# Kernel optimization log

Hardware: AMD Instinct MI355X
Metric: run time of the kernel (lower is better)

The kernel has to match this reference:

```python
import jax, jax.numpy as jnp
import numpy as np

B, M, N = 1, 128, 256          # batch, MSA rows, residues
C_IN, C_PAIR = 256, 128        # rep1d_feat, rep2d_feat
H, C = 8, 32                   # num_heads, attention_num_c
EPS = 1e-5


def layer_norm(x, g, b):
    mu = jnp.mean(x, axis=-1, keepdims=True)
    var = jnp.var(x, axis=-1, keepdims=True)
    return (x - mu) * jax.lax.rsqrt(var + EPS) * g + b


def setup_inputs() -> dict:
    key = jax.random.key(0)
    ks = jax.random.split(key, 10)
    s_in = 1.0 / np.sqrt(C_IN)
    s_pair = 1.0 / np.sqrt(C_PAIR)
    s_hc = 1.0 / np.sqrt(H * C)
    return {
        "x1d": jax.random.normal(ks[0], (B, M, N, C_IN), jnp.float32),
        "x2d": jax.random.normal(ks[1], (B, N, N, C_PAIR), jnp.float32),
        "ln1_g": jnp.ones((C_IN,), jnp.float32),
        "ln1_b": jnp.zeros((C_IN,), jnp.float32),
        "ln2_g": jnp.ones((C_PAIR,), jnp.float32),
        "ln2_b": jnp.zeros((C_PAIR,), jnp.float32),
        "Wq": jax.random.normal(ks[2], (C_IN, H * C), jnp.float32) * s_in,
        "Wk": jax.random.normal(ks[3], (C_IN, H * C), jnp.float32) * s_in,
        "Wv": jax.random.normal(ks[4], (C_IN, H * C), jnp.float32) * s_in,
        "W2d": jax.random.normal(ks[5], (C_PAIR, H), jnp.float32) * s_pair,
        "Wgate": jax.random.normal(ks[6], (C_IN, H * C), jnp.float32) * s_in,
        "bgate": jnp.zeros((H * C,), jnp.float32),
        "Wfinal": jax.random.normal(ks[7], (H * C, C_IN), jnp.float32) * s_hc,
        "bfinal": jnp.zeros((C_IN,), jnp.float32),
    }


def reference(x1d, x2d, ln1_g, ln1_b, ln2_g, ln2_b,
              Wq, Wk, Wv, W2d, Wgate, bgate, Wfinal, bfinal):
    x1 = layer_norm(x1d, ln1_g, ln1_b)                      # [b,m,i,c_in]
    x2 = layer_norm(x2d, ln2_g, ln2_b)                      # [b,i,j,c_pair]
    bias = jnp.einsum('bijp,ph->bhij', x2, W2d)             # [b,h,i,j]

    factor = 1.0 / np.sqrt(C).astype(np.float32)
    q = jnp.einsum('bmid,dhc->bmihc', x1, Wq.reshape(C_IN, H, C)) * factor
    k = jnp.einsum('bmid,dhc->bmihc', x1, Wk.reshape(C_IN, H, C))
    v = jnp.einsum('bmid,dhc->bmihc', x1, Wv.reshape(C_IN, H, C))

    aff = jnp.einsum('bmihc,bmjhc->bmhij', q, k)            # [b,m,h,i,j]
    weights = jax.nn.softmax(aff + bias[:, None], axis=-1)

    gate = jax.nn.sigmoid(
        jnp.einsum('bmid,dhc->bmihc', x1, Wgate.reshape(C_IN, H, C))
        + bgate.reshape(1, 1, 1, H, C))

    out = jnp.einsum('bmhqk,bmkhc->bmqhc', weights, v) * gate
    out = jnp.einsum('bmqhc,hcd->bmqd', out, Wfinal.reshape(H, C, C_IN)) + bfinal
    return out
```

## Files before the change

kernel.cpp:

```cpp
#include <hip/hip_runtime.h>


typedef unsigned short u16;
typedef unsigned int   u32;
typedef __attribute__((ext_vector_type(8))) __bf16 bf16x8;
typedef __attribute__((ext_vector_type(4))) float  f32x4;

#define DEV __device__ __forceinline__

DEV float bf2f(u16 s) {
    u32 u = ((u32)s) << 16;
    float f;
    __builtin_memcpy(&f, &u, 4);
    return f;
}
DEV u16 f2bf(float f) {
    u32 u;
    __builtin_memcpy(&u, &f, 4);
    u = (u + 0x7fffu + ((u >> 16) & 1u)) >> 16;
    return (u16)u;
}

#define GLD_LDS16(gp, lp)                                                           \
    __builtin_amdgcn_global_load_lds(                                               \
        (const __attribute__((address_space(1))) u32*)(const void*)(gp),            \
        (__attribute__((address_space(3))) u32*)(void*)(lp), 16, 0, 0)

__global__ void k_transpose(const float* __restrict__ Wq, const float* __restrict__ Wk,
                            const float* __restrict__ Wv, const float* __restrict__ Wg,
                            const float* __restrict__ Wf,
                            u16* __restrict__ WT, u16* __restrict__ WfT) {
    int idx = blockIdx.x * 256 + threadIdx.x;
    if (idx < 1024 * 256) {
        int gcol = idx >> 8, p = idx & 255;
        int sel = gcol >> 8, c = gcol & 255;
        const float* W = sel == 0 ? Wq : sel == 1 ? Wk : sel == 2 ? Wv : Wg;
        WT[idx] = f2bf(W[p * 256 + c]);
    } else {
        int j = idx - 1024 * 256;
        int d = j >> 8, hc = j & 255;
        WfT[j] = f2bf(Wf[hc * 256 + d]);
    }
}

__global__ __launch_bounds__(256) void k_ln1(const float* __restrict__ x,
                                             const float* __restrict__ gg,
                                             const float* __restrict__ bb,
                                             u16* __restrict__ y) {
    int lane = threadIdx.x & 63, wave = threadIdx.x >> 6;
    int row = blockIdx.x * 4 + wave;
    float4 xv = *(const float4*)(x + row * 256 + lane * 4);
    float v0 = xv.x, v1 = xv.y, v2 = xv.z, v3 = xv.w;
    float s  = v0 + v1 + v2 + v3;
    float s2 = v0*v0 + v1*v1 + v2*v2 + v3*v3;
    #pragma unroll
    for (int msk = 32; msk; msk >>= 1) {
        s  += __shfl_xor(s,  msk, 64);
        s2 += __shfl_xor(s2, msk, 64);
    }
    float mu  = s * (1.0f / 256.0f);
    float var = s2 * (1.0f / 256.0f) - mu * mu;
    float rs  = rsqrtf(var + 1e-5f);
    float4 gv = *(const float4*)(gg + lane * 4);
    float4 bv = *(const float4*)(bb + lane * 4);
    ushort4 o;
    o.x = f2bf((v0 - mu) * rs * gv.x + bv.x);
    o.y = f2bf((v1 - mu) * rs * gv.y + bv.y);
    o.z = f2bf((v2 - mu) * rs * gv.z + bv.z);
    o.w = f2bf((v3 - mu) * rs * gv.w + bv.w);
    *(ushort4*)(y + row * 256 + lane * 4) = o;
}

__global__ __launch_bounds__(256) void k_ln2bias(const float* __restrict__ x2,
                                                 const float* __restrict__ gg,
                                                 const float* __restrict__ bb,
                                                 const float* __restrict__ W2d,
                                                 float* __restrict__ bias) {
    int lane = threadIdx.x & 63, wave = threadIdx.x >> 6;
    int row = blockIdx.x * 4 + wave;
    float2 xv = *(const float2*)(x2 + row * 128 + lane * 2);
    float v0 = xv.x, v1 = xv.y;
    float s = v0 + v1, s2 = v0*v0 + v1*v1;
    #pragma unroll
    for (int msk = 32; msk; msk >>= 1) {
        s  += __shfl_xor(s,  msk, 64);
        s2 += __shfl_xor(s2, msk, 64);
    }
    float mu  = s * (1.0f / 128.0f);
    float var = s2 * (1.0f / 128.0f) - mu * mu;
    float rs  = rsqrtf(var + 1e-5f);
    float2 gv = *(const float2*)(gg + lane * 2);
    float2 bv = *(const float2*)(bb + lane * 2);
    float xn0 = (v0 - mu) * rs * gv.x + bv.x;
    float xn1 = (v1 - mu) * rs * gv.y + bv.y;
    int p0 = lane * 2;
    float4 w0a = *(const float4*)(W2d + p0 * 8);
    float4 w0b = *(const float4*)(W2d + p0 * 8 + 4);
    float4 w1a = *(const float4*)(W2d + (p0 + 1) * 8);
    float4 w1b = *(const float4*)(W2d + (p0 + 1) * 8 + 4);
    float p[8];
    p[0] = xn0 * w0a.x + xn1 * w1a.x;
    p[1] = xn0 * w0a.y + xn1 * w1a.y;
    p[2] = xn0 * w0a.z + xn1 * w1a.z;
    p[3] = xn0 * w0a.w + xn1 * w1a.w;
    p[4] = xn0 * w0b.x + xn1 * w1b.x;
    p[5] = xn0 * w0b.y + xn1 * w1b.y;
    p[6] = xn0 * w0b.z + xn1 * w1b.z;
    p[7] = xn0 * w0b.w + xn1 * w1b.w;
    #pragma unroll
    for (int hh = 0; hh < 8; hh++)
        #pragma unroll
        for (int msk = 32; msk; msk >>= 1)
            p[hh] += __shfl_xor(p[hh], msk, 64);
    if (lane == 0) {
        #pragma unroll
        for (int hh = 0; hh < 8; hh++)
            bias[hh * 65536 + row] = p[hh];
    }
}

DEV void gemm128_core(const u16* __restrict__ X, const u16* __restrict__ WTb,
                      int rowbase, int colbase, int K,
                      u16* As, u16* Bs, f32x4 acc[4][4], int lane, int wave) {
    int l8 = lane & 7, r8 = lane >> 3;
    int gchunk = l8 ^ (r8 & 7);
    int lrow = lane & 15, quad = lane >> 4;
    int wr = (wave >> 1) * 64, wc = (wave & 1) * 64;

    for (int kk = 0; kk < K; kk += 64) {
        #pragma unroll
        for (int i = 0; i < 4; i++) {
            int s = wave * 4 + i;
            const u16* g = X + (rowbase + s * 8 + r8) * K + kk + gchunk * 8;
            GLD_LDS16(g, As + s * 512);
        }
        #pragma unroll
        for (int i = 0; i < 4; i++) {
            int s = wave * 4 + i;
            const u16* g = WTb + (colbase + s * 8 + r8) * K + kk + gchunk * 8;
            GLD_LDS16(g, Bs + s * 512);
        }
        __syncthreads();
        #pragma unroll
        for (int k2 = 0; k2 < 64; k2 += 32) {
            int cidx = (k2 >> 3) + quad;
            bf16x8 af[4], bf[4];
            #pragma unroll
            for (int t = 0; t < 4; t++) {
                int R = wr + t * 16 + lrow;
                af[t] = *(const bf16x8*)(As + R * 64 + ((cidx ^ (R & 7)) << 3));
            }
            #pragma unroll
            for (int t = 0; t < 4; t++) {
                int R = wc + t * 16 + lrow;
                bf[t] = *(const bf16x8*)(Bs + R * 64 + ((cidx ^ (R & 7)) << 3));
            }
            #pragma unroll
            for (int i = 0; i < 4; i++)
                #pragma unroll
                for (int j = 0; j < 4; j++)
                    acc[i][j] = __builtin_amdgcn_mfma_f32_16x16x32_bf16(af[i], bf[j], acc[i][j], 0, 0, 0);
        }
        __syncthreads();
    }
}

__global__ __launch_bounds__(256) void k_qkvg(const u16* __restrict__ X, const u16* __restrict__ WT,
                                              u16* __restrict__ q, u16* __restrict__ kb,
                                              u16* __restrict__ vt, u16* __restrict__ gt,
                                              const float* __restrict__ bgate) {
    __shared__ u16 As[128 * 64];
    __shared__ u16 Bs[128 * 64];
    int lane = threadIdx.x & 63, wave = threadIdx.x >> 6;
    int rowbase = blockIdx.x * 128;
    int colbase = blockIdx.y * 128;
    f32x4 acc[4][4];
    #pragma unroll
    for (int i = 0; i < 4; i++)
        #pragma unroll
        for (int j = 0; j < 4; j++)
            acc[i][j] = (f32x4){0.f, 0.f, 0.f, 0.f};
    gemm128_core(X, WT, rowbase, colbase, 256, As, Bs, acc, lane, wave);
    int lrow = lane & 15, quad = lane >> 4;
    int wrb = rowbase + (wave >> 1) * 64, wcb = colbase + (wave & 1) * 64;
    int which = blockIdx.y >> 1;
    #pragma unroll
    for (int it = 0; it < 4; it++)
        #pragma unroll
        for (int jt = 0; jt < 4; jt++)
            #pragma unroll
            for (int r = 0; r < 4; r++) {
                int grow = wrb + it * 16 + quad * 4 + r;
                int gcol = wcb + jt * 16 + lrow;
                int o = gcol & 255;
                float v = acc[it][jt][r];
                if (which == 0) {
                    q[grow * 256 + o] = f2bf(v * 0.17677669529663687f);
                } else if (which == 1) {
                    kb[grow * 256 + o] = f2bf(v);
                } else if (which == 2) {
                    int mm = grow >> 8, ii = grow & 255;
                    vt[(mm * 256 + o) * 256 + ii] = f2bf(v);
                } else {
                    float z = v + bgate[o];
                    gt[grow * 256 + o] = f2bf(1.0f / (1.0f + __expf(-z)));
                }
            }
}

__global__ __launch_bounds__(256) void k_attn(const u16* __restrict__ q, const u16* __restrict__ kb,
                                              const u16* __restrict__ vt, const u16* __restrict__ gt,
                                              const float* __restrict__ bias,
                                              u16* __restrict__ tmp) {
    __shared__ u16 P[4][16][264];
    int lane = threadIdx.x & 63, wave = threadIdx.x >> 6;
    int lrow = lane & 15, quad = lane >> 4, lk = quad * 8;
    int m = blockIdx.x, h = blockIdx.y, iblk = blockIdx.z;
    int i0 = iblk * 64 + wave * 16;

    bf16x8 aq = *(const bf16x8*)(q + (m * 256 + i0 + lrow) * 256 + h * 32 + lk);
    f32x4 acc[16];
    #pragma unroll
    for (int jt = 0; jt < 16; jt++) {
        bf16x8 bk = *(const bf16x8*)(kb + (m * 256 + jt * 16 + lrow) * 256 + h * 32 + lk);
        f32x4 z = {0.f, 0.f, 0.f, 0.f};
        acc[jt] = __builtin_amdgcn_mfma_f32_16x16x32_bf16(aq, bk, z, 0, 0, 0);
    }

    float rmax[4] = {-1e30f, -1e30f, -1e30f, -1e30f};
    #pragma unroll
    for (int jt = 0; jt < 16; jt++)
        #pragma unroll
        for (int r = 0; r < 4; r++) {
            int i = i0 + quad * 4 + r;
            int j = jt * 16 + lrow;
            float a = acc[jt][r] + bias[h * 65536 + i * 256 + j];
            acc[jt][r] = a;
            rmax[r] = fmaxf(rmax[r], a);
        }
    #pragma unroll
    for (int r = 0; r < 4; r++)
        #pragma unroll
        for (int msk = 8; msk; msk >>= 1)
            rmax[r] = fmaxf(rmax[r], __shfl_xor(rmax[r], msk, 64));
    float rsum[4] = {0.f, 0.f, 0.f, 0.f};
    #pragma unroll
    for (int jt = 0; jt < 16; jt++)
        #pragma unroll
        for (int r = 0; r < 4; r++) {
            float e = __expf(acc[jt][r] - rmax[r]);
            acc[jt][r] = e;
            rsum[r] += e;
        }
    #pragma unroll
    for (int r = 0; r < 4; r++) {
        #pragma unroll
        for (int msk = 8; msk; msk >>= 1)
            rsum[r] += __shfl_xor(rsum[r], msk, 64);
        rsum[r] = 1.0f / fmaxf(rsum[r], 1e-30f);
    }

    #pragma unroll
    for (int jt = 0; jt < 16; jt++)
        #pragma unroll
        for (int r = 0; r < 4; r++)
            P[wave][quad * 4 + r][jt * 16 + lrow] = f2bf(acc[jt][r] * rsum[r]);
    __syncthreads();

    f32x4 oacc[2] = {{0.f,0.f,0.f,0.f}, {0.f,0.f,0.f,0.f}};
    const u16* Pw = &P[wave][0][0];
    for (int kk2 = 0; kk2 < 256; kk2 += 32) {
        bf16x8 ap = *(const bf16x8*)(Pw + lrow * 264 + kk2 + lk);
        #pragma unroll
        for (int ct = 0; ct < 2; ct++) {
            bf16x8 bv = *(const bf16x8*)(vt + (m * 256 + h * 32 + ct * 16 + lrow) * 256 + kk2 + lk);
            oacc[ct] = __builtin_amdgcn_mfma_f32_16x16x32_bf16(ap, bv, oacc[ct], 0, 0, 0);
        }
    }

    #pragma unroll
    for (int ct = 0; ct < 2; ct++)
        #pragma unroll
        for (int r = 0; r < 4; r++) {
            int i = i0 + quad * 4 + r;
            int o = h * 32 + ct * 16 + lrow;
            float gv = bf2f(gt[(m * 256 + i) * 256 + o]);
            tmp[(m * 256 + i) * 256 + o] = f2bf(oacc[ct][r] * gv);
        }
}

__global__ __launch_bounds__(256) void k_final(const u16* __restrict__ T, const u16* __restrict__ WfT,
                                               const float* __restrict__ bfinal, float* __restrict__ out) {
    __shared__ u16 As[128 * 64];
    __shared__ u16 Bs[128 * 64];
    int lane = threadIdx.x & 63, wave = threadIdx.x >> 6;
    int rowbase = blockIdx.x * 128;
    int colbase = blockIdx.y * 128;
    f32x4 acc[4][4];
    #pragma unroll
    for (int i = 0; i < 4; i++)
        #pragma unroll
        for (int j = 0; j < 4; j++)
            acc[i][j] = (f32x4){0.f, 0.f, 0.f, 0.f};
    gemm128_core(T, WfT, rowbase, colbase, 256, As, Bs, acc, lane, wave);
    int lrow = lane & 15, quad = lane >> 4;
    int wrb = rowbase + (wave >> 1) * 64, wcb = colbase + (wave & 1) * 64;
    #pragma unroll
    for (int it = 0; it < 4; it++)
        #pragma unroll
        for (int jt = 0; jt < 4; jt++)
            #pragma unroll
            for (int r = 0; r < 4; r++) {
                int grow = wrb + it * 16 + quad * 4 + r;
                int gcol = wcb + jt * 16 + lrow;
                out[grow * 256 + gcol] = acc[it][jt][r] + bfinal[gcol];
            }
}

extern "C" void kernel_launch(void* const* d_in, const int* in_sizes, int n_in,
                              void* d_out, int out_size, void* d_ws, size_t ws_size,
                              hipStream_t stream) {
    const float* x1d   = (const float*)d_in[0];
    const float* x2d   = (const float*)d_in[1];
    const float* ln1_g = (const float*)d_in[2];
    const float* ln1_b = (const float*)d_in[3];
    const float* ln2_g = (const float*)d_in[4];
    const float* ln2_b = (const float*)d_in[5];
    const float* Wq    = (const float*)d_in[6];
    const float* Wk    = (const float*)d_in[7];
    const float* Wv    = (const float*)d_in[8];
    const float* W2d   = (const float*)d_in[9];
    const float* Wg    = (const float*)d_in[10];
    const float* bg    = (const float*)d_in[11];
    const float* Wf    = (const float*)d_in[12];
    const float* bfin  = (const float*)d_in[13];
    float* out = (float*)d_out;

    char* ws = (char*)d_ws;
    u16*   x1   = (u16*)(ws);
    u16*   WT   = (u16*)(ws + 16777216);
    u16*   WfT  = (u16*)(ws + 17301504);
    float* bias = (float*)(ws + 17432576);
    u16*   qb   = (u16*)(ws + 19529728);
    u16*   kb   = (u16*)(ws + 36306944);
    u16*   vtb  = (u16*)(ws + 53084160);
    u16*   gb   = (u16*)(ws + 69861376);
    u16*   tmp  = x1;

    k_transpose<<<1280, 256, 0, stream>>>(Wq, Wk, Wv, Wg, Wf, WT, WfT);
    k_ln1<<<8192, 256, 0, stream>>>(x1d, ln1_g, ln1_b, x1);
    k_ln2bias<<<16384, 256, 0, stream>>>(x2d, ln2_g, ln2_b, W2d, bias);
    k_qkvg<<<dim3(256, 8), 256, 0, stream>>>(x1, WT, qb, kb, vtb, gb, bg);
    k_attn<<<dim3(128, 8, 4), 256, 0, stream>>>(qb, kb, vtb, gb, bias, tmp);
    k_final<<<dim3(256, 2), 256, 0, stream>>>(tmp, WfT, bfin, out);
}
```

Measured before the change: 312.8 us.

## Loop query tiles per block, transpose bias layout, vectorize gated output

The attention kernel now launches one block per (m,h) and has each wave loop over four 16-row query tiles, reusing the same K/V slice from cache instead of spreading rows across four z-blocks. The bias is stored transposed so each lane reads four consecutive i values as one float4. The PV MFMA operands are swapped so each lane's outputs are contiguous, which allows ushort4 gate loads and output stores. It also drops the __syncthreads, since each wave only touches its own P buffer. The cost is four times fewer blocks, which lowers parallelism and latency hiding, and the tile loop runs serially inside each wave.

```diff
diff --git a/kernel.cpp b/kernel.cpp
--- a/kernel.cpp
+++ b/kernel.cpp
@@ -113,9 +113,10 @@
         for (int msk = 32; msk; msk >>= 1)
             p[hh] += __shfl_xor(p[hh], msk, 64);
     if (lane == 0) {
+        int i = row >> 8, j = row & 255;
         #pragma unroll
         for (int hh = 0; hh < 8; hh++)
-            bias[hh * 65536 + row] = p[hh];
+            bias[hh * 65536 + j * 256 + i] = p[hh];
     }
 }
 
@@ -215,78 +216,83 @@
     __shared__ u16 P[4][16][264];
     int lane = threadIdx.x & 63, wave = threadIdx.x >> 6;
     int lrow = lane & 15, quad = lane >> 4, lk = quad * 8;
-    int m = blockIdx.x, h = blockIdx.y, iblk = blockIdx.z;
-    int i0 = iblk * 64 + wave * 16;
-
-    bf16x8 aq = *(const bf16x8*)(q + (m * 256 + i0 + lrow) * 256 + h * 32 + lk);
-    f32x4 acc[16];
-    #pragma unroll
-    for (int jt = 0; jt < 16; jt++) {
-        bf16x8 bk = *(const bf16x8*)(kb + (m * 256 + jt * 16 + lrow) * 256 + h * 32 + lk);
-        f32x4 z = {0.f, 0.f, 0.f, 0.f};
-        acc[jt] = __builtin_amdgcn_mfma_f32_16x16x32_bf16(aq, bk, z, 0, 0, 0);
-    }
-
-    float rmax[4] = {-1e30f, -1e30f, -1e30f, -1e30f};
-    #pragma unroll
-    for (int jt = 0; jt < 16; jt++)
+    int m = blockIdx.x, h = blockIdx.y;
+    const u16* kslice = kb + (m * 256) * 256 + h * 32;
+    const u16* vslice = vt + (m * 256 + h * 32) * 256;
+    const float* bslice = bias + h * 65536;
+    u16* Pw = &P[wave][0][0];
+
+    for (int t = 0; t < 4; t++) {
+        int i0 = wave * 64 + t * 16;
+
+        bf16x8 aq = *(const bf16x8*)(q + (m * 256 + i0 + lrow) * 256 + h * 32 + lk);
+        f32x4 acc[16];
+        #pragma unroll
+        for (int jt = 0; jt < 16; jt++) {
+            bf16x8 bk = *(const bf16x8*)(kslice + (jt * 16 + lrow) * 256 + lk);
+            f32x4 z = {0.f, 0.f, 0.f, 0.f};
+            acc[jt] = __builtin_amdgcn_mfma_f32_16x16x32_bf16(aq, bk, z, 0, 0, 0);
+        }
+
+        float rmax[4] = {-1e30f, -1e30f, -1e30f, -1e30f};
+        #pragma unroll
+        for (int jt = 0; jt < 16; jt++) {
+            float4 b4 = *(const float4*)(bslice + (jt * 16 + lrow) * 256 + i0 + quad * 4);
+            acc[jt][0] += b4.x;  acc[jt][1] += b4.y;
+            acc[jt][2] += b4.z;  acc[jt][3] += b4.w;
+            #pragma unroll
+            for (int r = 0; r < 4; r++) rmax[r] = fmaxf(rmax[r], acc[jt][r]);
+        }
+        #pragma unroll
+        for (int r = 0; r < 4; r++)
+            #pragma unroll
+            for (int msk = 8; msk; msk >>= 1)
+                rmax[r] = fmaxf(rmax[r], __shfl_xor(rmax[r], msk, 64));
+        float rsum[4] = {0.f, 0.f, 0.f, 0.f};
+        #pragma unroll
+        for (int jt = 0; jt < 16; jt++)
+            #pragma unroll
+            for (int r = 0; r < 4; r++) {
+                float e = __expf(acc[jt][r] - rmax[r]);
+                acc[jt][r] = e;
+                rsum[r] += e;
+            }
         #pragma unroll
         for (int r = 0; r < 4; r++) {
-            int i = i0 + quad * 4 + r;
-            int j = jt * 16 + lrow;
-            float a = acc[jt][r] + bias[h * 65536 + i * 256 + j];
-            acc[jt][r] = a;
-            rmax[r] = fmaxf(rmax[r], a);
-        }
-    #pragma unroll
-    for (int r = 0; r < 4; r++)
-        #pragma unroll
-        for (int msk = 8; msk; msk >>= 1)
-            rmax[r] = fmaxf(rmax[r], __shfl_xor(rmax[r], msk, 64));
-    float rsum[4] = {0.f, 0.f, 0.f, 0.f};
-    #pragma unroll
-    for (int jt = 0; jt < 16; jt++)
-        #pragma unroll
-        for (int r = 0; r < 4; r++) {
-            float e = __expf(acc[jt][r] - rmax[r]);
-            acc[jt][r] = e;
-            rsum[r] += e;
-        }
-    #pragma unroll
-    for (int r = 0; r < 4; r++) {
-        #pragma unroll
-        for (int msk = 8; msk; msk >>= 1)
-            rsum[r] += __shfl_xor(rsum[r], msk, 64);
-        rsum[r] = 1.0f / fmaxf(rsum[r], 1e-30f);
-    }
-
-    #pragma unroll
-    for (int jt = 0; jt < 16; jt++)
-        #pragma unroll
-        for (int r = 0; r < 4; r++)
-            P[wave][quad * 4 + r][jt * 16 + lrow] = f2bf(acc[jt][r] * rsum[r]);
-    __syncthreads();
-
-    f32x4 oacc[2] = {{0.f,0.f,0.f,0.f}, {0.f,0.f,0.f,0.f}};
-    const u16* Pw = &P[wave][0][0];
-    for (int kk2 = 0; kk2 < 256; kk2 += 32) {
-        bf16x8 ap = *(const bf16x8*)(Pw + lrow * 264 + kk2 + lk);
+            #pragma unroll
+            for (int msk = 8; msk; msk >>= 1)
+                rsum[r] += __shfl_xor(rsum[r], msk, 64);
+            rsum[r] = 1.0f / fmaxf(rsum[r], 1e-30f);
+        }
+
+        #pragma unroll
+        for (int jt = 0; jt < 16; jt++)
+            #pragma unroll
+            for (int r = 0; r < 4; r++)
+                Pw[(quad * 4 + r) * 264 + jt * 16 + lrow] = f2bf(acc[jt][r] * rsum[r]);
+
+        f32x4 oacc[2] = {{0.f,0.f,0.f,0.f}, {0.f,0.f,0.f,0.f}};
+        for (int kk2 = 0; kk2 < 256; kk2 += 32) {
+            bf16x8 bp = *(const bf16x8*)(Pw + lrow * 264 + kk2 + lk);
+            #pragma unroll
+            for (int ct = 0; ct < 2; ct++) {
+                bf16x8 av = *(const bf16x8*)(vslice + (ct * 16 + lrow) * 256 + kk2 + lk);
+                oacc[ct] = __builtin_amdgcn_mfma_f32_16x16x32_bf16(av, bp, oacc[ct], 0, 0, 0);
+            }
+        }
+
         #pragma unroll
         for (int ct = 0; ct < 2; ct++) {
-            bf16x8 bv = *(const bf16x8*)(vt + (m * 256 + h * 32 + ct * 16 + lrow) * 256 + kk2 + lk);
-            oacc[ct] = __builtin_amdgcn_mfma_f32_16x16x32_bf16(ap, bv, oacc[ct], 0, 0, 0);
-        }
-    }
-
-    #pragma unroll
-    for (int ct = 0; ct < 2; ct++)
-        #pragma unroll
-        for (int r = 0; r < 4; r++) {
-            int i = i0 + quad * 4 + r;
-            int o = h * 32 + ct * 16 + lrow;
-            float gv = bf2f(gt[(m * 256 + i) * 256 + o]);
-            tmp[(m * 256 + i) * 256 + o] = f2bf(oacc[ct][r] * gv);
-        }
+            int base = (m * 256 + i0 + lrow) * 256 + h * 32 + ct * 16 + quad * 4;
+            ushort4 g4 = *(const ushort4*)(gt + base);
+            ushort4 o4;
+            o4.x = f2bf(oacc[ct][0] * bf2f(g4.x));
+            o4.y = f2bf(oacc[ct][1] * bf2f(g4.y));
+            o4.z = f2bf(oacc[ct][2] * bf2f(g4.z));
+            o4.w = f2bf(oacc[ct][3] * bf2f(g4.w));
+            *(ushort4*)(tmp + base) = o4;
+        }
+    }
 }
 
 __global__ __launch_bounds__(256) void k_final(const u16* __restrict__ T, const u16* __restrict__ WfT,
@@ -351,6 +357,6 @@
     k_ln1<<<8192, 256, 0, stream>>>(x1d, ln1_g, ln1_b, x1);
     k_ln2bias<<<16384, 256, 0, stream>>>(x2d, ln2_g, ln2_b, W2d, bias);
     k_qkvg<<<dim3(256, 8), 256, 0, stream>>>(x1, WT, qb, kb, vtb, gb, bg);
-    k_attn<<<dim3(128, 8, 4), 256, 0, stream>>>(qb, kb, vtb, gb, bias, tmp);
+    k_attn<<<dim3(128, 8), 256, 0, stream>>>(qb, kb, vtb, gb, bias, tmp);
     k_final<<<dim3(256, 2), 256, 0, stream>>>(tmp, WfT, bfin, out);
 }
```

New measurement: 315.7 us. No clear change (+0.9%).

## Tile weight transpose through LDS, reorder attention grid, drop per-wave barrier

Applied to the files above, without the earlier changes.

The weight transpose now stages 64x64 tiles in padded shared memory, so both the global reads and the bf16 writes are coalesced, and it needs far fewer blocks. The attention grid is reordered so the four i-blocks of the same (m,h) run next to each other, which is meant to improve L2 reuse of K and V. It also adds a launch-bounds occupancy hint. The __syncthreads after writing P is removed because each wave reads only its own P slice. That relies on intra-wave ordering of LDS accesses, which normally holds on a single wavefront.

```diff
diff --git a/kernel.cpp b/kernel.cpp
--- a/kernel.cpp
+++ b/kernel.cpp
@@ -26,20 +26,28 @@
         (const __attribute__((address_space(1))) u32*)(const void*)(gp),            \
         (__attribute__((address_space(3))) u32*)(void*)(lp), 16, 0, 0)
 
-__global__ void k_transpose(const float* __restrict__ Wq, const float* __restrict__ Wk,
+__global__ __launch_bounds__(256) void k_transpose(const float* __restrict__ Wq, const float* __restrict__ Wk,
                             const float* __restrict__ Wv, const float* __restrict__ Wg,
                             const float* __restrict__ Wf,
                             u16* __restrict__ WT, u16* __restrict__ WfT) {
-    int idx = blockIdx.x * 256 + threadIdx.x;
-    if (idx < 1024 * 256) {
-        int gcol = idx >> 8, p = idx & 255;
-        int sel = gcol >> 8, c = gcol & 255;
-        const float* W = sel == 0 ? Wq : sel == 1 ? Wk : sel == 2 ? Wv : Wg;
-        WT[idx] = f2bf(W[p * 256 + c]);
-    } else {
-        int j = idx - 1024 * 256;
-        int d = j >> 8, hc = j & 255;
-        WfT[j] = f2bf(Wf[hc * 256 + d]);
+    __shared__ float T[64][65];
+    int b = blockIdx.x;
+    int mat = b >> 4, tile = b & 15;
+    int p0 = (tile & 3) * 64, c0 = (tile >> 2) * 64;
+    const float* W = mat == 0 ? Wq : mat == 1 ? Wk : mat == 2 ? Wv : mat == 3 ? Wg : Wf;
+    u16* outp = (mat < 4) ? (WT + mat * 256 * 256) : WfT;
+    int tr = threadIdx.x >> 6;
+    int tc = threadIdx.x & 63;
+    #pragma unroll
+    for (int rr = 0; rr < 16; rr++) {
+        int r = rr * 4 + tr;
+        T[r][tc] = W[(p0 + r) * 256 + c0 + tc];
+    }
+    __syncthreads();
+    #pragma unroll
+    for (int rr = 0; rr < 16; rr++) {
+        int r = rr * 4 + tr;
+        outp[(c0 + r) * 256 + p0 + tc] = f2bf(T[tc][r]);
     }
 }
 
@@ -208,14 +216,14 @@
             }
 }
 
-__global__ __launch_bounds__(256) void k_attn(const u16* __restrict__ q, const u16* __restrict__ kb,
+__global__ __launch_bounds__(256, 5) void k_attn(const u16* __restrict__ q, const u16* __restrict__ kb,
                                               const u16* __restrict__ vt, const u16* __restrict__ gt,
                                               const float* __restrict__ bias,
                                               u16* __restrict__ tmp) {
     __shared__ u16 P[4][16][264];
     int lane = threadIdx.x & 63, wave = threadIdx.x >> 6;
     int lrow = lane & 15, quad = lane >> 4, lk = quad * 8;
-    int m = blockIdx.x, h = blockIdx.y, iblk = blockIdx.z;
+    int iblk = blockIdx.x, m = blockIdx.y, h = blockIdx.z;
     int i0 = iblk * 64 + wave * 16;
 
     bf16x8 aq = *(const bf16x8*)(q + (m * 256 + i0 + lrow) * 256 + h * 32 + lk);
@@ -265,7 +273,6 @@
         #pragma unroll
         for (int r = 0; r < 4; r++)
             P[wave][quad * 4 + r][jt * 16 + lrow] = f2bf(acc[jt][r] * rsum[r]);
-    __syncthreads();
 
     f32x4 oacc[2] = {{0.f,0.f,0.f,0.f}, {0.f,0.f,0.f,0.f}};
     const u16* Pw = &P[wave][0][0];
@@ -347,10 +354,10 @@
     u16*   gb   = (u16*)(ws + 69861376);
     u16*   tmp  = x1;
 
-    k_transpose<<<1280, 256, 0, stream>>>(Wq, Wk, Wv, Wg, Wf, WT, WfT);
+    k_transpose<<<80, 256, 0, stream>>>(Wq, Wk, Wv, Wg, Wf, WT, WfT);
     k_ln1<<<8192, 256, 0, stream>>>(x1d, ln1_g, ln1_b, x1);
     k_ln2bias<<<16384, 256, 0, stream>>>(x2d, ln2_g, ln2_b, W2d, bias);
     k_qkvg<<<dim3(256, 8), 256, 0, stream>>>(x1, WT, qb, kb, vtb, gb, bg);
-    k_attn<<<dim3(128, 8, 4), 256, 0, stream>>>(qb, kb, vtb, gb, bias, tmp);
+    k_attn<<<dim3(4, 128, 8), 256, 0, stream>>>(qb, kb, vtb, gb, bias, tmp);
     k_final<<<dim3(256, 2), 256, 0, stream>>>(tmp, WfT, bfin, out);
 }
```

Result: no change. 316.0 us (+1.0%).
